# Kernel tuning notes

Measured on AMD Instinct MI355X. Metric: run time of the kernel, lower is better.

## Reference

```python
import jax, jax.numpy as jnp
import numpy as np
import math

D_MODEL = 512
D_FF = 4 * D_MODEL
N_EXPERTS = 8
VOCAB = 256
TOL = 0.15          # TeslaHarmonicGate tolerance
HARM = math.pi / 3.0  # harmonic spacing (Tesla 3-6-9 -> pi*k/3 harmonics over [-pi, pi])


def tesla_gate(angle):
    # Snap angle to the nearest harmonic (multiple of pi/3) when within tolerance.
    nearest = jnp.round(angle / HARM) * HARM
    return jnp.where(jnp.abs(angle - nearest) < TOL, nearest, angle)


def setup_inputs() -> dict:
    key = jax.random.key(0)
    ks = jax.random.split(key, 16)
    s = lambda d: 1.0 / np.sqrt(d)
    return {
        "byte_seq": jax.random.randint(ks[0], (4, 2048), 0, VOCAB, dtype=jnp.int32),
        "emb":    jax.random.normal(ks[1], (VOCAB, D_MODEL), jnp.float32) * 0.02,
        "phi_w":  jax.random.normal(ks[2], (D_MODEL, D_MODEL), jnp.float32) * s(D_MODEL),
        "phi_b":  jnp.zeros((D_MODEL,), jnp.float32),
        "amp_w":  jax.random.normal(ks[3], (D_MODEL, D_MODEL), jnp.float32) * s(D_MODEL),
        "amp_b":  jnp.zeros((D_MODEL,), jnp.float32),
        "gate_w": jax.random.normal(ks[4], (D_MODEL, N_EXPERTS), jnp.float32) * s(D_MODEL),
        "gate_b": jnp.zeros((N_EXPERTS,), jnp.float32),
        "w1":     jax.random.normal(ks[5], (N_EXPERTS, D_MODEL, D_FF), jnp.float32) * s(D_MODEL),
        "b1":     jnp.zeros((N_EXPERTS, D_FF), jnp.float32),
        "w2":     jax.random.normal(ks[6], (N_EXPERTS, D_FF, D_MODEL), jnp.float32) * s(D_FF),
        "b2":     jnp.zeros((N_EXPERTS, D_MODEL), jnp.float32),
        "head_w": jax.random.normal(ks[7], (D_MODEL, VOCAB), jnp.float32) * s(D_MODEL),
        "head_b": jnp.zeros((VOCAB,), jnp.float32),
    }


def _toroidal(x, phi_w, phi_b, amp_w, amp_b):
    # x: [B, T, C]; sequential toroidal recurrence over T via lax.scan.
    B, T, C = x.shape
    state0 = jnp.zeros((B, C), x.dtype)

    def step(state, xt):  # xt: [B, C]
        raw_angle = jnp.tanh(xt @ phi_w + phi_b) * jnp.pi
        angle = tesla_gate(raw_angle)
        new_state = jnp.cos(angle) * state - jnp.sin(angle) * (1.0 - state)
        new_state = jnp.clip(new_state, -1.0, 1.0)
        gated = jax.nn.sigmoid(xt @ amp_w + amp_b) * new_state
        return new_state, gated

    final_state, out = jax.lax.scan(step, state0, jnp.swapaxes(x, 0, 1))
    return jnp.swapaxes(out, 0, 1), final_state  # [B,T,C], [B,C]


def _moe(x, gate_w, gate_b, w1, b1, w2, b2):
    # Top-2 softmax routing with renormalized weights; per-expert FFN (GELU).
    B, T, C = x.shape
    xt = x.reshape(B * T, C)                        # [N, C]
    probs = jax.nn.softmax(xt @ gate_w + gate_b)    # [N, E]
    topw, topi = jax.lax.top_k(probs, 2)            # [N, 2]
    topw = topw / jnp.sum(topw, axis=-1, keepdims=True)
    out = jnp.zeros_like(xt)
    for e in range(N_EXPERTS):  # fixed small expert loop
        w_e = jnp.sum(jnp.where(topi == e, topw, 0.0), axis=-1)  # [N]
        h = jax.nn.gelu(xt @ w1[e] + b1[e])
        out = out + w_e[:, None] * (h @ w2[e] + b2[e])
    return out.reshape(B, T, C)


def reference(byte_seq, emb, phi_w, phi_b, amp_w, amp_b, gate_w, gate_b,
              w1, b1, w2, b2, head_w, head_b):
    x = emb[byte_seq]                                  # [B, T, C]
    x, next_state = _toroidal(x, phi_w, phi_b, amp_w, amp_b)
    moe_out = _moe(x, gate_w, gate_b, w1, b1, w2, b2)
    logits = moe_out @ head_w + head_b                 # [B, T, 256]
    return logits, next_state
```

## Files before the change

### kernel.cpp

```cpp
#include <hip/hip_runtime.h>
#include <hip/hip_fp16.h>
#include <math.h>


#define PI_F 3.14159265358979323846f
#define HARM_F 1.04719755119659774615f
#define INV_HARM_F 0.95492965855137201461f
#define TOL_F 0.15f

typedef float f32x16 __attribute__((ext_vector_type(16)));
typedef __bf16 bf16x8 __attribute__((ext_vector_type(8)));
typedef unsigned int u32x4 __attribute__((ext_vector_type(4)));
typedef unsigned int u32x2 __attribute__((ext_vector_type(2)));

__device__ __forceinline__ float bflo(unsigned u) { return __uint_as_float(u << 16); }
__device__ __forceinline__ float bfhi(unsigned u) { return __uint_as_float(u & 0xFFFF0000u); }
__device__ __forceinline__ unsigned short f2bf(float x) {
  unsigned u = __float_as_uint(x);
  unsigned r = (u + 0x7FFFu + ((u >> 16) & 1u)) >> 16;
  return (unsigned short)r;
}
__device__ __forceinline__ bf16x8 ld_frag(const void* p) {
  u32x4 v = *(const u32x4*)p;
  return __builtin_bit_cast(bf16x8, v);
}
__device__ __forceinline__ float tanh_fast(float z) {
  float zc = fminf(10.f, fmaxf(-10.f, z));
  float e2 = __expf(zc + zc);
  return (e2 - 1.f) / (e2 + 1.f);
}
__device__ __forceinline__ float sigmoid_fast(float z) {
  return 1.f / (1.f + __expf(-z));
}
__device__ __forceinline__ float gelu_tanh(float x) {
  float x3 = x * x * x;
  float t = 0.79788456080286535588f * (x + 0.044715f * x3);
  return 0.5f * x * (1.f + tanh_fast(t));
}
__device__ __forceinline__ void sincos_poly(float a, float* sn, float* cs) {
  float q = rintf(a * 0.63661977236758134f);
  int iq = (int)q;
  float t = fmaf(-q, 1.57079637050628662f, a);
  t = fmaf(q, 4.37113883e-8f, t);
  float t2 = t * t;
  float sp = t * fmaf(t2, fmaf(t2, fmaf(t2, -1.9515296e-4f, 8.3321609e-3f),
                               -1.6666654e-1f), 1.f);
  float cp = fmaf(t2 * t2,
                  fmaf(t2, fmaf(t2, 2.4433158e-5f, -1.3887316e-3f), 4.1666646e-2f),
                  fmaf(t2, -0.5f, 1.f));
  int m = iq & 3;
  bool swap = (m & 1) != 0;
  float ss = swap ? cp : sp;
  float cc = swap ? sp : cp;
  *sn = (m & 2) ? -ss : ss;
  *cs = ((m + 1) & 2) ? -cc : cc;
}

__global__ void k_embed2(const int* __restrict__ seq, const float* __restrict__ emb,
                         unsigned short* __restrict__ XhiP,
                         unsigned short* __restrict__ XloP) {
  int gid = blockIdx.x * 256 + threadIdx.x;
  int ent = gid >> 6, l = gid & 63;
  int tb = ent >> 5, ks = ent & 31;
  int tok = tb * 32 + (l & 31);
  int k0 = ks * 16 + (l >> 5) * 8;
  const float* src = emb + (size_t)seq[tok] * 512 + k0;
  float4 v0 = *(const float4*)src;
  float4 v1 = *(const float4*)(src + 4);
  float vv[8] = {v0.x, v0.y, v0.z, v0.w, v1.x, v1.y, v1.z, v1.w};
  unsigned h[8], lo[8];
#pragma unroll
  for (int j = 0; j < 8; ++j) {
    h[j] = f2bf(vv[j]);
    lo[j] = f2bf(vv[j] - bflo(h[j]));
  }
  u32x4 H, L;
  H.x = h[0] | (h[1] << 16);  H.y = h[2] | (h[3] << 16);
  H.z = h[4] | (h[5] << 16);  H.w = h[6] | (h[7] << 16);
  L.x = lo[0] | (lo[1] << 16); L.y = lo[2] | (lo[3] << 16);
  L.z = lo[4] | (lo[5] << 16); L.w = lo[6] | (lo[7] << 16);
  *(u32x4*)(XhiP + (size_t)ent * 512 + l * 8) = H;
  *(u32x4*)(XloP + (size_t)ent * 512 + l * 8) = L;
}

__global__ __launch_bounds__(256) void k_pack_b(const float* __restrict__ src, int ld,
                                                size_t srcE, unsigned short* __restrict__ dst,
                                                size_t dstE, int fragKtot) {
  __shared__ float Ls[512 * 33];
  int nb = blockIdx.x, kseg = blockIdx.y, e = blockIdx.z;
  const float* s = src + (size_t)e * srcE + (size_t)kseg * 512 * ld + nb * 32;
  unsigned short* d = dst + (size_t)e * dstE + ((size_t)(nb * fragKtot + kseg * 32)) * 512;
  int tid = threadIdx.x;
#pragma unroll
  for (int q = 0; q < 16; ++q) {
    int i = tid + q * 256;
    int row = i >> 3, c4 = i & 7;
    float4 v = *(const float4*)(s + (size_t)row * ld + c4 * 4);
    Ls[row * 33 + c4 * 4 + 0] = v.x;
    Ls[row * 33 + c4 * 4 + 1] = v.y;
    Ls[row * 33 + c4 * 4 + 2] = v.z;
    Ls[row * 33 + c4 * 4 + 3] = v.w;
  }
  __syncthreads();
#pragma unroll
  for (int q = 0; q < 8; ++q) {
    int i = tid + q * 256;
    int ks = i >> 6, l = i & 63;
    int col = l & 31, kb = (l >> 5) * 8 + ks * 16;
    u32x4 o;
    o.x = (unsigned)f2bf(Ls[(kb + 0) * 33 + col]) | ((unsigned)f2bf(Ls[(kb + 1) * 33 + col]) << 16);
    o.y = (unsigned)f2bf(Ls[(kb + 2) * 33 + col]) | ((unsigned)f2bf(Ls[(kb + 3) * 33 + col]) << 16);
    o.z = (unsigned)f2bf(Ls[(kb + 4) * 33 + col]) | ((unsigned)f2bf(Ls[(kb + 5) * 33 + col]) << 16);
    o.w = (unsigned)f2bf(Ls[(kb + 6) * 33 + col]) | ((unsigned)f2bf(Ls[(kb + 7) * 33 + col]) << 16);
    *(u32x4*)(d + (size_t)ks * 512 + l * 8) = o;
  }
}

__global__ __launch_bounds__(256, 3) void k_phi(
    const unsigned short* __restrict__ XhiP, const unsigned short* __restrict__ XloP,
    const float* __restrict__ phiW, const float* __restrict__ phiB,
    const float* __restrict__ ampW, const float* __restrict__ ampB,
    float* __restrict__ cosO, float* __restrict__ sinO, float* __restrict__ sigO) {
  __shared__ __align__(16) char wlds[2][8][1024];
  int tid = threadIdx.x;
  int w = tid >> 6, l = tid & 63;
  int l31 = l & 31, hi = l >> 5;
  int by = blockIdx.y;
  const float* Bsrc = (by < 4) ? phiW : ampW;
  const float* bias = (by < 4) ? phiB : ampB;
  int cb = (by & 3) * 128;

#define STAGE_W(KS, BUF)                                                        \
  {                                                                             \
    const float* wsrc = Bsrc + (size_t)((KS)*16 + hi * 8) * 512 + cb + w * 32 + l31; \
    float v0 = wsrc[0],    v1 = wsrc[512],  v2 = wsrc[1024], v3 = wsrc[1536];   \
    float v4 = wsrc[2048], v5 = wsrc[2560], v6 = wsrc[3072], v7 = wsrc[3584];   \
    unsigned h0 = f2bf(v0), h1 = f2bf(v1), h2 = f2bf(v2), h3 = f2bf(v3);        \
    unsigned h4 = f2bf(v4), h5 = f2bf(v5), h6 = f2bf(v6), h7 = f2bf(v7);        \
    u32x4 H, L;                                                                 \
    H.x = h0 | (h1 << 16); H.y = h2 | (h3 << 16);                               \
    H.z = h4 | (h5 << 16); H.w = h6 | (h7 << 16);                               \
    L.x = (unsigned)f2bf(v0 - bflo(h0)) | ((unsigned)f2bf(v1 - bflo(h1)) << 16); \
    L.y = (unsigned)f2bf(v2 - bflo(h2)) | ((unsigned)f2bf(v3 - bflo(h3)) << 16); \
    L.z = (unsigned)f2bf(v4 - bflo(h4)) | ((unsigned)f2bf(v5 - bflo(h5)) << 16); \
    L.w = (unsigned)f2bf(v6 - bflo(h6)) | ((unsigned)f2bf(v7 - bflo(h7)) << 16); \
    *(u32x4*)(&wlds[BUF][w * 2 + 0][l * 16]) = H;                               \
    *(u32x4*)(&wlds[BUF][w * 2 + 1][l * 16]) = L;                               \
  }

  int tb = blockIdx.x * 4 + w;
  const unsigned short* xh_base = XhiP + ((size_t)tb * 32) * 512 + l * 8;
  const unsigned short* xl_base = XloP + ((size_t)tb * 32) * 512 + l * 8;
  f32x16 a0, a1, a2, a3;
#pragma unroll
  for (int i = 0; i < 16; ++i) { a0[i] = 0.f; a1[i] = 0.f; a2[i] = 0.f; a3[i] = 0.f; }

  STAGE_W(0, 0);
  for (int ks = 0; ks < 32; ++ks) {
    __syncthreads();
    if (ks + 1 < 32) {
      if (((ks + 1) & 1) == 0) STAGE_W(ks + 1, 0) else STAGE_W(ks + 1, 1)
    }
    bf16x8 xh = *(const bf16x8*)(xh_base + (size_t)ks * 512);
    bf16x8 xl = *(const bf16x8*)(xl_base + (size_t)ks * 512);
    const char (*wb)[1024] = wlds[ks & 1];
    bf16x8 wh0 = ld_frag(&wb[0][l * 16]), wl0 = ld_frag(&wb[1][l * 16]);
    bf16x8 wh1 = ld_frag(&wb[2][l * 16]), wl1 = ld_frag(&wb[3][l * 16]);
    bf16x8 wh2 = ld_frag(&wb[4][l * 16]), wl2 = ld_frag(&wb[5][l * 16]);
    bf16x8 wh3 = ld_frag(&wb[6][l * 16]), wl3 = ld_frag(&wb[7][l * 16]);
    a0 = __builtin_amdgcn_mfma_f32_32x32x16_bf16(xh, wh0, a0, 0, 0, 0);
    a1 = __builtin_amdgcn_mfma_f32_32x32x16_bf16(xh, wh1, a1, 0, 0, 0);
    a2 = __builtin_amdgcn_mfma_f32_32x32x16_bf16(xh, wh2, a2, 0, 0, 0);
    a3 = __builtin_amdgcn_mfma_f32_32x32x16_bf16(xh, wh3, a3, 0, 0, 0);
    a0 = __builtin_amdgcn_mfma_f32_32x32x16_bf16(xl, wh0, a0, 0, 0, 0);
    a1 = __builtin_amdgcn_mfma_f32_32x32x16_bf16(xl, wh1, a1, 0, 0, 0);
    a2 = __builtin_amdgcn_mfma_f32_32x32x16_bf16(xl, wh2, a2, 0, 0, 0);
    a3 = __builtin_amdgcn_mfma_f32_32x32x16_bf16(xl, wh3, a3, 0, 0, 0);
    a0 = __builtin_amdgcn_mfma_f32_32x32x16_bf16(xh, wl0, a0, 0, 0, 0);
    a1 = __builtin_amdgcn_mfma_f32_32x32x16_bf16(xh, wl1, a1, 0, 0, 0);
    a2 = __builtin_amdgcn_mfma_f32_32x32x16_bf16(xh, wl2, a2, 0, 0, 0);
    a3 = __builtin_amdgcn_mfma_f32_32x32x16_bf16(xh, wl3, a3, 0, 0, 0);
  }

  int tokBase = blockIdx.x * 128 + w * 32;
#define PHI_EPI(ACC, NB)                                                        \
  {                                                                             \
    int c = cb + (NB)*32 + l31;                                                 \
    float bs = bias[c];                                                         \
    if (by < 4) {                                                               \
      _Pragma("unroll") for (int r = 0; r < 16; ++r) {                          \
        int tok = tokBase + (r & 3) + 8 * (r >> 2) + 4 * hi;                    \
        float z = ACC[r] + bs;                                                  \
        float a = tanh_fast(z) * PI_F;                                          \
        float nr = rintf(a * INV_HARM_F) * HARM_F;                              \
        if (fabsf(a - nr) < TOL_F) a = nr;                                      \
        float sn, cs;                                                           \
        sincos_poly(a, &sn, &cs);                                               \
        cosO[(size_t)tok * 512 + c] = cs;                                       \
        sinO[(size_t)tok * 512 + c] = sn;                                       \
      }                                                                         \
    } else {                                                                    \
      _Pragma("unroll") for (int r = 0; r < 16; ++r) {                          \
        int tok = tokBase + (r & 3) + 8 * (r >> 2) + 4 * hi;                    \
        sigO[(size_t)tok * 512 + c] = sigmoid_fast(ACC[r] + bs);                \
      }                                                                         \
    }                                                                           \
  }
  PHI_EPI(a0, 0)
  PHI_EPI(a1, 1)
  PHI_EPI(a2, 2)
  PHI_EPI(a3, 3)
}

__global__ __launch_bounds__(256, 1) void k_scan(const float* __restrict__ cosb,
                                                 const float* __restrict__ sinb,
                                                 const float* __restrict__ sigb,
                                                 float* __restrict__ xmoe,
                                                 float* __restrict__ nstate) {
  __shared__ float lds[2][3][64 * 64];
  int tid = threadIdx.x;
  int wv = tid >> 6, l = tid & 63;
  int b = blockIdx.x >> 3;
  int c0 = (blockIdx.x & 7) << 6;
  size_t base = ((size_t)b * 2048) * 512 + c0;

#define SCAN_STAGE(SRC, K, BUF)                                                \
  {                                                                            \
    float4 tmp[16];                                                            \
    size_t sb = base + ((size_t)(K) * 64 + tq) * 512 + cq * 4;                 \
    _Pragma("unroll") for (int t4 = 0; t4 < 16; ++t4)                          \
      tmp[t4] = *(const float4*)((SRC) + sb + (size_t)t4 * 4 * 512);           \
    _Pragma("unroll") for (int t4 = 0; t4 < 16; ++t4)                          \
      *(float4*)(&lds[BUF][wv - 1][(t4 * 4 + tq) * 64 + cq * 4]) = tmp[t4];    \
  }

  if (wv > 0) {
    const float* src = (wv == 1) ? cosb : (wv == 2) ? sinb : sigb;
    int tq = l >> 4, cq = l & 15;
    SCAN_STAGE(src, 0, 0);
    __syncthreads();
    for (int k = 0; k < 32; ++k) {
      if (k + 1 < 32) {
        if (((k + 1) & 1) == 0) SCAN_STAGE(src, k + 1, 0)
        else                    SCAN_STAGE(src, k + 1, 1)
      }
      __syncthreads();
    }
  } else {
    __syncthreads();
    float state = 0.f;
    for (int k = 0; k < 32; ++k) {
      const float* bufC = &lds[k & 1][0][0];
      const float* bufS = &lds[k & 1][1][0];
      const float* bufG = &lds[k & 1][2][0];
      size_t outb = base + (size_t)k * 64 * 512 + l;
#pragma unroll
      for (int tt = 0; tt < 64; ++tt) {
        float pc = bufC[tt * 64 + l];
        float ps = bufS[tt * 64 + l];
        float pg = bufG[tt * 64 + l];
        float st = fmaf(pc + ps, state, -ps);
        st = fminf(1.f, fmaxf(-1.f, st));
        state = st;
        xmoe[outb + (size_t)tt * 512] = pg * st;
      }
      __syncthreads();
    }
    nstate[(size_t)b * 512 + c0 + l] = state;
  }
}

__global__ __launch_bounds__(256) void k_gate(const float* __restrict__ xmoe,
                                              const float* __restrict__ gw_g,
                                              const float* __restrict__ gb,
                                              int* __restrict__ e01p,
                                              unsigned* __restrict__ w01p) {
  __shared__ float gw[4096];
  int tid = threadIdx.x;
  for (int i = tid; i < 4096; i += 256) gw[i] = gw_g[i];
  __syncthreads();
  int tok = blockIdx.x * 32 + (tid >> 3);
  int e = tid & 7;
  float acc = gb[e];
  const float4* xr = (const float4*)(xmoe + (size_t)tok * 512);
  for (int k4 = 0; k4 < 128; ++k4) {
    float4 x = xr[k4];
    acc += x.x * gw[(k4 * 4 + 0) * 8 + e];
    acc += x.y * gw[(k4 * 4 + 1) * 8 + e];
    acc += x.z * gw[(k4 * 4 + 2) * 8 + e];
    acc += x.w * gw[(k4 * 4 + 3) * 8 + e];
  }
  float m = acc;
  m = fmaxf(m, __shfl_xor(m, 1));
  m = fmaxf(m, __shfl_xor(m, 2));
  m = fmaxf(m, __shfl_xor(m, 4));
  float p = expf(acc - m);
  float ss = p;
  ss += __shfl_xor(ss, 1); ss += __shfl_xor(ss, 2); ss += __shfl_xor(ss, 4);
  p /= ss;
  float v1 = p; int i1 = e;
  {
    float ov; int oi;
    ov = __shfl_xor(v1, 1); oi = __shfl_xor(i1, 1);
    if (ov > v1 || (ov == v1 && oi < i1)) { v1 = ov; i1 = oi; }
    ov = __shfl_xor(v1, 2); oi = __shfl_xor(i1, 2);
    if (ov > v1 || (ov == v1 && oi < i1)) { v1 = ov; i1 = oi; }
    ov = __shfl_xor(v1, 4); oi = __shfl_xor(i1, 4);
    if (ov > v1 || (ov == v1 && oi < i1)) { v1 = ov; i1 = oi; }
  }
  float v2 = (e == i1) ? -1.f : p; int i2 = e;
  {
    float ov; int oi;
    ov = __shfl_xor(v2, 1); oi = __shfl_xor(i2, 1);
    if (ov > v2 || (ov == v2 && oi < i2)) { v2 = ov; i2 = oi; }
    ov = __shfl_xor(v2, 2); oi = __shfl_xor(i2, 2);
    if (ov > v2 || (ov == v2 && oi < i2)) { v2 = ov; i2 = oi; }
    ov = __shfl_xor(v2, 4); oi = __shfl_xor(i2, 4);
    if (ov > v2 || (ov == v2 && oi < i2)) { v2 = ov; i2 = oi; }
  }
  if (e == 0) {
    float s2 = v1 + v2;
    __half h1 = __float2half(v1 / s2), h2 = __float2half(v2 / s2);
    e01p[tok] = i1 | (i2 << 8);
    w01p[tok] = (unsigned)__half_as_ushort(h1) | ((unsigned)__half_as_ushort(h2) << 16);
  }
}

__global__ void k_build(const int* __restrict__ e01p, const unsigned* __restrict__ w01p,
                        int* __restrict__ list, float* __restrict__ wlist,
                        int* __restrict__ counts, int* __restrict__ eoff,
                        int* __restrict__ tokpos, int* __restrict__ tmap) {
  __shared__ int cnt[8], cur[8];
  int tid = threadIdx.x, lane = tid & 63;
  if (tid < 8) cnt[tid] = 0;
  __syncthreads();
  for (int i = tid; i < 16384; i += 256) {
    int tok = i >> 1, j = i & 1;
    int ee = (e01p[tok] >> (8 * j)) & 255;
#pragma unroll
    for (int x = 0; x < 8; ++x) {
      unsigned long long m = __ballot(ee == x);
      if (m != 0ull && lane == (__ffsll((long long)m) - 1)) atomicAdd(&cnt[x], __popcll(m));
    }
  }
  __syncthreads();
  if (tid == 0) {
    int s = 0;
#pragma unroll
    for (int x = 0; x < 8; ++x) {
      cur[x] = s; eoff[x] = s; counts[x] = cnt[x]; s += cnt[x];
    }
  }
  __syncthreads();
  for (int i = tid; i < 272; i += 256) tmap[i] = -1;
  __syncthreads();
  if (tid == 0) {
    int ntiles = 0, tstart[8];
#pragma unroll
    for (int e = 0; e < 8; ++e) { tstart[e] = ntiles; ntiles += (cnt[e] + 95) / 96; }
    int q = ntiles >> 3, r = ntiles & 7;
    for (int e = 0; e < 8; ++e) {
      int nt = (cnt[e] + 95) / 96;
      for (int t = 0; t < nt; ++t) {
        int k = tstart[e] + t;
        int c, o;
        if (k < r * (q + 1)) { c = k / (q + 1); o = k - c * (q + 1); }
        else { int k2 = k - r * (q + 1); c = r + k2 / q; o = k2 - (k2 / q) * q; }
        tmap[8 * o + c] = (e << 16) | t;
      }
    }
  }
  __syncthreads();
  for (int i = tid; i < 16384; i += 256) {
    int tok = i >> 1, j = i & 1;
    int ee = (e01p[tok] >> (8 * j)) & 255;
    unsigned wp = w01p[tok];
    unsigned short us = (unsigned short)(j ? (wp >> 16) : (wp & 0xFFFFu));
    float w = __half2float(__ushort_as_half(us));
    int pos = 0;
#pragma unroll
    for (int x = 0; x < 8; ++x) {
      unsigned long long m = __ballot(ee == x);
      if (m == 0ull) continue;
      int leader = __ffsll((long long)m) - 1;
      int bb = 0;
      if (lane == leader) bb = atomicAdd(&cur[x], __popcll(m));
      bb = __shfl(bb, leader);
      if (ee == x) pos = bb + __popcll(m & ((1ull << lane) - 1ull));
    }
    list[pos] = tok;
    wlist[pos] = w;
    tokpos[i] = pos;
  }
}

#define HS_OFF 98304

__global__ __launch_bounds__(512, 2) void k_ffn(
    const float* __restrict__ xmoe, const int* __restrict__ list,
    const float* __restrict__ wlist, const int* __restrict__ counts,
    const int* __restrict__ eoff, const int* __restrict__ tmap,
    const unsigned short* __restrict__ W1Pk, const float* __restrict__ b1g,
    const unsigned short* __restrict__ W2Pk, const float* __restrict__ b2g,
    unsigned short* __restrict__ Yb) {
  int mp = tmap[blockIdx.x];
  if (mp < 0) return;
  int e = mp >> 16, tile = mp & 0xFFFF;
  int cnt = counts[e];
  int base = eoff[e] + tile * 96;
  int valid = cnt - tile * 96;
  if (valid > 96) valid = 96;
  __shared__ __align__(16) char smem[147456];
  __shared__ int toks[96];
  __shared__ float wts[96];
  int tid = threadIdx.x;
  int w = tid >> 6, l = tid & 63;
  int l31 = l & 31, hi = l >> 5;
  if (tid < 96) {
    int idx = tile * 96 + tid;
    bool v = idx < cnt;
    toks[tid] = list[eoff[e] + (v ? idx : 0)];
    wts[tid] = v ? wlist[eoff[e] + idx] : 0.f;
  }
  __syncthreads();
#pragma unroll
  for (int s = 0; s < 12; ++s) {
    int sl = s * 512 + tid;
    int ent = sl >> 6, ll = sl & 63;
    int ks = ent / 3, t3 = ent - ks * 3;
    int tok = toks[t3 * 32 + (ll & 31)];
    const float* src = xmoe + (size_t)tok * 512 + ks * 16 + (ll >> 5) * 8;
    float4 v0 = *(const float4*)src;
    float4 v1 = *(const float4*)(src + 4);
    u32x4 u;
    u.x = (unsigned)f2bf(v0.x) | ((unsigned)f2bf(v0.y) << 16);
    u.y = (unsigned)f2bf(v0.z) | ((unsigned)f2bf(v0.w) << 16);
    u.z = (unsigned)f2bf(v1.x) | ((unsigned)f2bf(v1.y) << 16);
    u.w = (unsigned)f2bf(v1.z) | ((unsigned)f2bf(v1.w) << 16);
    *(u32x4*)(smem + ent * 1024 + ll * 16) = u;
  }
  f32x16 acc00, acc01, acc02, acc10, acc11, acc12;
#pragma unroll
  for (int i = 0; i < 16; ++i) {
    acc00[i] = 0.f; acc01[i] = 0.f; acc02[i] = 0.f;
    acc10[i] = 0.f; acc11[i] = 0.f; acc12[i] = 0.f;
  }
  __syncthreads();

  const size_t dstE1 = (size_t)64 * 32 * 512;
  const size_t dstE2 = (size_t)16 * 128 * 512;
  for (int it = 0; it < 8; ++it) {
    f32x16 z0, z1, z2;
#pragma unroll
    for (int i = 0; i < 16; ++i) { z0[i] = 0.f; z1[i] = 0.f; z2[i] = 0.f; }
    const unsigned short* w1p =
        W1Pk + (size_t)e * dstE1 + ((size_t)(it * 8 + w) * 32) * 512 + l * 8;
#pragma unroll 8
    for (int ks = 0; ks < 32; ++ks) {
      bf16x8 a = *(const bf16x8*)(w1p + (size_t)ks * 512);
      bf16x8 b0 = ld_frag(smem + (ks * 3 + 0) * 1024 + l * 16);
      bf16x8 b1 = ld_frag(smem + (ks * 3 + 1) * 1024 + l * 16);
      bf16x8 b2 = ld_frag(smem + (ks * 3 + 2) * 1024 + l * 16);
      z0 = __builtin_amdgcn_mfma_f32_32x32x16_bf16(a, b0, z0, 0, 0, 0);
      z1 = __builtin_amdgcn_mfma_f32_32x32x16_bf16(a, b1, z1, 0, 0, 0);
      z2 = __builtin_amdgcn_mfma_f32_32x32x16_bf16(a, b2, z2, 0, 0, 0);
    }
#define GELU_STORE(Z, T3)                                                       \
  {                                                                             \
    _Pragma("unroll") for (int rq = 0; rq < 4; ++rq) {                          \
      int fb = w * 32 + 8 * rq + 4 * hi;                                        \
      float4 bv = *(const float4*)(b1g + e * 2048 + it * 256 + fb);             \
      float g0 = gelu_tanh(Z[4 * rq + 0] + bv.x);                               \
      float g1 = gelu_tanh(Z[4 * rq + 1] + bv.y);                               \
      float g2 = gelu_tanh(Z[4 * rq + 2] + bv.z);                               \
      float g3 = gelu_tanh(Z[4 * rq + 3] + bv.w);                               \
      u32x2 p;                                                                  \
      p.x = (unsigned)f2bf(g0) | ((unsigned)f2bf(g1) << 16);                    \
      p.y = (unsigned)f2bf(g2) | ((unsigned)f2bf(g3) << 16);                    \
      int ent = (w * 2 + (rq >> 1)) * 3 + (T3);                                 \
      int lanep = l31 + 32 * (rq & 1);                                          \
      *(u32x2*)(smem + HS_OFF + ent * 1024 + lanep * 16 + hi * 8) = p;          \
    }                                                                           \
  }
    GELU_STORE(z0, 0)
    GELU_STORE(z1, 1)
    GELU_STORE(z2, 2)
    __syncthreads();
    const unsigned short* w2a =
        W2Pk + (size_t)e * dstE2 + ((size_t)(w * 2) * 128 + it * 16) * 512 + l * 8;
    const unsigned short* w2b = w2a + (size_t)128 * 512;
#pragma unroll 8
    for (int fs = 0; fs < 16; ++fs) {
      bf16x8 a0 = *(const bf16x8*)(w2a + (size_t)fs * 512);
      bf16x8 a1 = *(const bf16x8*)(w2b + (size_t)fs * 512);
      bf16x8 h0 = ld_frag(smem + HS_OFF + (fs * 3 + 0) * 1024 + l * 16);
      bf16x8 h1 = ld_frag(smem + HS_OFF + (fs * 3 + 1) * 1024 + l * 16);
      bf16x8 h2 = ld_frag(smem + HS_OFF + (fs * 3 + 2) * 1024 + l * 16);
      acc00 = __builtin_amdgcn_mfma_f32_32x32x16_bf16(a0, h0, acc00, 0, 0, 0);
      acc01 = __builtin_amdgcn_mfma_f32_32x32x16_bf16(a0, h1, acc01, 0, 0, 0);
      acc02 = __builtin_amdgcn_mfma_f32_32x32x16_bf16(a0, h2, acc02, 0, 0, 0);
      acc10 = __builtin_amdgcn_mfma_f32_32x32x16_bf16(a1, h0, acc10, 0, 0, 0);
      acc11 = __builtin_amdgcn_mfma_f32_32x32x16_bf16(a1, h1, acc11, 0, 0, 0);
      acc12 = __builtin_amdgcn_mfma_f32_32x32x16_bf16(a1, h2, acc12, 0, 0, 0);
    }
    __syncthreads();
  }
#define EPI_STORE(ACC, JC, T3)                                                  \
  {                                                                             \
    _Pragma("unroll") for (int rq = 0; rq < 4; ++rq) {                          \
      int c0 = (w * 2 + (JC)) * 32 + 8 * rq + 4 * hi;                           \
      float4 b2v = *(const float4*)(b2g + e * 512 + c0);                        \
      int tok = (T3)*32 + l31;                                                  \
      float wt = wts[tok];                                                      \
      u32x2 p;                                                                  \
      p.x = (unsigned)f2bf((ACC[4 * rq + 0] + b2v.x) * wt) |                    \
            ((unsigned)f2bf((ACC[4 * rq + 1] + b2v.y) * wt) << 16);             \
      p.y = (unsigned)f2bf((ACC[4 * rq + 2] + b2v.z) * wt) |                    \
            ((unsigned)f2bf((ACC[4 * rq + 3] + b2v.w) * wt) << 16);             \
      *(u32x2*)(smem + tok * 1024 + ((c0 * 2) ^ ((tok & 7) << 4))) = p;         \
    }                                                                           \
  }
  EPI_STORE(acc00, 0, 0)
  EPI_STORE(acc01, 0, 1)
  EPI_STORE(acc02, 0, 2)
  EPI_STORE(acc10, 1, 0)
  EPI_STORE(acc11, 1, 1)
  EPI_STORE(acc12, 1, 2)
  __syncthreads();
#pragma unroll
  for (int s = 0; s < 12; ++s) {
    int i = tid + s * 512;
    int row = i >> 6, g = i & 63;
    if (row < valid) {
      u32x4 v = *(u32x4*)(smem + row * 1024 + ((g * 16) ^ ((row & 7) << 4)));
      *(u32x4*)(Yb + (size_t)(base + row) * 512 + g * 8) = v;
    }
  }
}

__global__ __launch_bounds__(256) void k_head(const unsigned short* __restrict__ Yb,
                                              const int* __restrict__ tokpos,
                                              const unsigned short* __restrict__ headPk,
                                              const float* __restrict__ headB,
                                              float* __restrict__ out) {
  __shared__ __align__(16) char As[16384];
  __shared__ int tp[256];
  int tid = threadIdx.x;
  int w = tid >> 6, l = tid & 63;
  int l31 = l & 31, hi = l >> 5;
  int mg = w & 1, ng = w >> 1;
  int bm = blockIdx.x * 128, by = blockIdx.y;
  tp[tid] = tokpos[bm * 2 + tid];
  f32x16 acc00, acc01, acc10, acc11;
#pragma unroll
  for (int i = 0; i < 16; ++i) { acc00[i] = 0.f; acc01[i] = 0.f; acc10[i] = 0.f; acc11[i] = 0.f; }
  int nblk0 = by * 4 + ng * 2;
  __syncthreads();
  for (int kb = 0; kb < 8; ++kb) {
#pragma unroll
    for (int s = 0; s < 4; ++s) {
      int i = tid + s * 256;
      int row = i >> 3, g = i & 7;
      int p1 = tp[row * 2], p2 = tp[row * 2 + 1];
      u32x4 va = *(const u32x4*)(Yb + (size_t)p1 * 512 + kb * 64 + g * 8);
      u32x4 vb = *(const u32x4*)(Yb + (size_t)p2 * 512 + kb * 64 + g * 8);
      u32x4 o;
      o.x = (unsigned)f2bf(bflo(va.x) + bflo(vb.x)) | ((unsigned)f2bf(bfhi(va.x) + bfhi(vb.x)) << 16);
      o.y = (unsigned)f2bf(bflo(va.y) + bflo(vb.y)) | ((unsigned)f2bf(bfhi(va.y) + bfhi(vb.y)) << 16);
      o.z = (unsigned)f2bf(bflo(va.z) + bflo(vb.z)) | ((unsigned)f2bf(bfhi(va.z) + bfhi(vb.z)) << 16);
      o.w = (unsigned)f2bf(bflo(va.w) + bflo(vb.w)) | ((unsigned)f2bf(bfhi(va.w) + bfhi(vb.w)) << 16);
      *(u32x4*)(As + row * 128 + ((g * 16) ^ ((row & 7) << 4))) = o;
    }
    __syncthreads();
#pragma unroll
    for (int ks = 0; ks < 4; ++ks) {
      int r0 = mg * 64 + l31, r1 = r0 + 32;
      int kbyte = ks * 32 + hi * 16;
      bf16x8 a0 = ld_frag(As + r0 * 128 + (kbyte ^ ((r0 & 7) << 4)));
      bf16x8 a1 = ld_frag(As + r1 * 128 + (kbyte ^ ((r1 & 7) << 4)));
      const unsigned short* hp = headPk + ((size_t)nblk0 * 32 + kb * 4 + ks) * 512 + l * 8;
      bf16x8 b0 = *(const bf16x8*)hp;
      bf16x8 b1 = *(const bf16x8*)(hp + 32 * 512);
      acc00 = __builtin_amdgcn_mfma_f32_32x32x16_bf16(a0, b0, acc00, 0, 0, 0);
      acc01 = __builtin_amdgcn_mfma_f32_32x32x16_bf16(a0, b1, acc01, 0, 0, 0);
      acc10 = __builtin_amdgcn_mfma_f32_32x32x16_bf16(a1, b0, acc10, 0, 0, 0);
      acc11 = __builtin_amdgcn_mfma_f32_32x32x16_bf16(a1, b1, acc11, 0, 0, 0);
    }
    __syncthreads();
  }
#pragma unroll
  for (int mf = 0; mf < 2; ++mf) {
#pragma unroll
    for (int nf = 0; nf < 2; ++nf) {
      int nc = by * 128 + ng * 64 + nf * 32 + l31;
      float hb = headB[nc];
#pragma unroll
      for (int r = 0; r < 16; ++r) {
        int m = bm + mg * 64 + mf * 32 + (r & 3) + 8 * (r >> 2) + 4 * hi;
        float v;
        if (mf == 0) v = (nf == 0) ? acc00[r] : acc01[r];
        else         v = (nf == 0) ? acc10[r] : acc11[r];
        out[(size_t)m * 256 + nc] = v + hb;
      }
    }
  }
}

extern "C" void kernel_launch(void* const* d_in, const int* in_sizes, int n_in,
                              void* d_out, int out_size, void* d_ws, size_t ws_size,
                              hipStream_t stream) {
  (void)in_sizes; (void)n_in; (void)out_size; (void)ws_size;
  const int* seq     = (const int*)d_in[0];
  const float* emb   = (const float*)d_in[1];
  const float* phi_w = (const float*)d_in[2];
  const float* phi_b = (const float*)d_in[3];
  const float* amp_w = (const float*)d_in[4];
  const float* amp_b = (const float*)d_in[5];
  const float* gate_w = (const float*)d_in[6];
  const float* gate_b = (const float*)d_in[7];
  const float* w1 = (const float*)d_in[8];
  const float* b1 = (const float*)d_in[9];
  const float* w2 = (const float*)d_in[10];
  const float* b2 = (const float*)d_in[11];
  const float* head_w = (const float*)d_in[12];
  const float* head_b = (const float*)d_in[13];
  float* out = (float*)d_out;

  char* ws = (char*)d_ws;
  const size_t BUF = 16777216;
  float* X    = (float*)(ws);
  float* COSb = (float*)(ws + BUF);
  float* SINb = (float*)(ws + 2 * BUF);
  float* SIGb = (float*)(ws + 3 * BUF);
  unsigned short* XhiP = (unsigned short*)X;
  unsigned short* XloP = XhiP + (size_t)8192 * 512;
  unsigned short* Yb   = (unsigned short*)COSb;
  unsigned short* W1Pk = (unsigned short*)SINb;
  unsigned short* W2Pk = (unsigned short*)SIGb;
  char* sm = ws + 4 * BUF;
  int*      e01p   = (int*)(sm);
  unsigned* w01p   = (unsigned*)(sm + 32768);
  int*      list   = (int*)(sm + 65536);
  float*    wlist  = (float*)(sm + 131072);
  int*      tokpos = (int*)(sm + 196608);
  int*      counts = (int*)(sm + 262144);
  int*      eoff   = (int*)(sm + 262144 + 64);
  unsigned short* headPk = (unsigned short*)(sm + 266240);
  int*      tmap   = (int*)(sm + 266240 + 262144);

  k_embed2<<<2048, 256, 0, stream>>>(seq, emb, XhiP, XloP);
  k_pack_b<<<dim3(8, 1, 1), 256, 0, stream>>>(head_w, 256, 0, headPk, 0, 32);
  k_phi<<<dim3(64, 8), 256, 0, stream>>>(XhiP, XloP, phi_w, phi_b, amp_w, amp_b,
                                         COSb, SINb, SIGb);
  k_scan<<<32, 256, 0, stream>>>(COSb, SINb, SIGb, X, out + 2097152);
  k_pack_b<<<dim3(64, 1, 8), 256, 0, stream>>>(w1, 2048, (size_t)512 * 2048, W1Pk,
                                               (size_t)64 * 32 * 512, 32);
  k_pack_b<<<dim3(16, 4, 8), 256, 0, stream>>>(w2, 512, (size_t)2048 * 512, W2Pk,
                                               (size_t)16 * 128 * 512, 128);
  k_gate<<<256, 256, 0, stream>>>(X, gate_w, gate_b, e01p, w01p);
  k_build<<<1, 256, 0, stream>>>(e01p, w01p, list, wlist, counts, eoff, tokpos, tmap);
  k_ffn<<<192, 512, 0, stream>>>(X, list, wlist, counts, eoff, tmap,
                                 W1Pk, b1, W2Pk, b2, Yb);
  k_head<<<dim3(64, 2), 256, 0, stream>>>(Yb, tokpos, headPk, head_b, out);
}
```

Before: 393.5 us.

## Split MoE FFN token groups across wave pairs with 1024-thread blocks

The expert FFN kernel now launches 1024 threads per block instead of 512, pairing waves so each pair splits the three 32-token groups. One wave handles two groups in the first GEMM and one in the second, and the other wave takes the opposite split, which balances MFMA work. The aim is to double resident waves per CU and cut per-wave accumulator registers, improving latency hiding on a grid of only 192 blocks. In exchange, each weight fragment is now loaded from global memory by both waves of a pair, and barriers now synchronize twice as many waves.

```diff
diff --git a/kernel.cpp b/kernel.cpp
--- a/kernel.cpp
+++ b/kernel.cpp
@@ -396,7 +396,7 @@
 
 #define HS_OFF 98304
 
-__global__ __launch_bounds__(512, 2) void k_ffn(
+__global__ __launch_bounds__(1024, 4) void k_ffn(
     const float* __restrict__ xmoe, const int* __restrict__ list,
     const float* __restrict__ wlist, const int* __restrict__ counts,
     const int* __restrict__ eoff, const int* __restrict__ tmap,
@@ -416,6 +416,7 @@
   int tid = threadIdx.x;
   int w = tid >> 6, l = tid & 63;
   int l31 = l & 31, hi = l >> 5;
+  int grp = w >> 1, fg = w & 1;
   if (tid < 96) {
     int idx = tile * 96 + tid;
     bool v = idx < cnt;
@@ -424,8 +425,8 @@
   }
   __syncthreads();
 #pragma unroll
-  for (int s = 0; s < 12; ++s) {
-    int sl = s * 512 + tid;
+  for (int s = 0; s < 6; ++s) {
+    int sl = s * 1024 + tid;
     int ent = sl >> 6, ll = sl & 63;
     int ks = ent / 3, t3 = ent - ks * 3;
     int tok = toks[t3 * 32 + (ll & 31)];
@@ -439,36 +440,15 @@
     u.w = (unsigned)f2bf(v1.z) | ((unsigned)f2bf(v1.w) << 16);
     *(u32x4*)(smem + ent * 1024 + ll * 16) = u;
   }
-  f32x16 acc00, acc01, acc02, acc10, acc11, acc12;
-#pragma unroll
-  for (int i = 0; i < 16; ++i) {
-    acc00[i] = 0.f; acc01[i] = 0.f; acc02[i] = 0.f;
-    acc10[i] = 0.f; acc11[i] = 0.f; acc12[i] = 0.f;
-  }
   __syncthreads();
 
   const size_t dstE1 = (size_t)64 * 32 * 512;
   const size_t dstE2 = (size_t)16 * 128 * 512;
-  for (int it = 0; it < 8; ++it) {
-    f32x16 z0, z1, z2;
-#pragma unroll
-    for (int i = 0; i < 16; ++i) { z0[i] = 0.f; z1[i] = 0.f; z2[i] = 0.f; }
-    const unsigned short* w1p =
-        W1Pk + (size_t)e * dstE1 + ((size_t)(it * 8 + w) * 32) * 512 + l * 8;
-#pragma unroll 8
-    for (int ks = 0; ks < 32; ++ks) {
-      bf16x8 a = *(const bf16x8*)(w1p + (size_t)ks * 512);
-      bf16x8 b0 = ld_frag(smem + (ks * 3 + 0) * 1024 + l * 16);
-      bf16x8 b1 = ld_frag(smem + (ks * 3 + 1) * 1024 + l * 16);
-      bf16x8 b2 = ld_frag(smem + (ks * 3 + 2) * 1024 + l * 16);
-      z0 = __builtin_amdgcn_mfma_f32_32x32x16_bf16(a, b0, z0, 0, 0, 0);
-      z1 = __builtin_amdgcn_mfma_f32_32x32x16_bf16(a, b1, z1, 0, 0, 0);
-      z2 = __builtin_amdgcn_mfma_f32_32x32x16_bf16(a, b2, z2, 0, 0, 0);
-    }
+
 #define GELU_STORE(Z, T3)                                                       \
   {                                                                             \
     _Pragma("unroll") for (int rq = 0; rq < 4; ++rq) {                          \
-      int fb = w * 32 + 8 * rq + 4 * hi;                                        \
+      int fb = grp * 32 + 8 * rq + 4 * hi;                                      \
       float4 bv = *(const float4*)(b1g + e * 2048 + it * 256 + fb);             \
       float g0 = gelu_tanh(Z[4 * rq + 0] + bv.x);                               \
       float g1 = gelu_tanh(Z[4 * rq + 1] + bv.y);                               \
@@ -477,38 +457,15 @@
       u32x2 p;                                                                  \
       p.x = (unsigned)f2bf(g0) | ((unsigned)f2bf(g1) << 16);                    \
       p.y = (unsigned)f2bf(g2) | ((unsigned)f2bf(g3) << 16);                    \
-      int ent = (w * 2 + (rq >> 1)) * 3 + (T3);                                 \
+      int ent = (grp * 2 + (rq >> 1)) * 3 + (T3);                               \
       int lanep = l31 + 32 * (rq & 1);                                          \
       *(u32x2*)(smem + HS_OFF + ent * 1024 + lanep * 16 + hi * 8) = p;          \
     }                                                                           \
   }
-    GELU_STORE(z0, 0)
-    GELU_STORE(z1, 1)
-    GELU_STORE(z2, 2)
-    __syncthreads();
-    const unsigned short* w2a =
-        W2Pk + (size_t)e * dstE2 + ((size_t)(w * 2) * 128 + it * 16) * 512 + l * 8;
-    const unsigned short* w2b = w2a + (size_t)128 * 512;
-#pragma unroll 8
-    for (int fs = 0; fs < 16; ++fs) {
-      bf16x8 a0 = *(const bf16x8*)(w2a + (size_t)fs * 512);
-      bf16x8 a1 = *(const bf16x8*)(w2b + (size_t)fs * 512);
-      bf16x8 h0 = ld_frag(smem + HS_OFF + (fs * 3 + 0) * 1024 + l * 16);
-      bf16x8 h1 = ld_frag(smem + HS_OFF + (fs * 3 + 1) * 1024 + l * 16);
-      bf16x8 h2 = ld_frag(smem + HS_OFF + (fs * 3 + 2) * 1024 + l * 16);
-      acc00 = __builtin_amdgcn_mfma_f32_32x32x16_bf16(a0, h0, acc00, 0, 0, 0);
-      acc01 = __builtin_amdgcn_mfma_f32_32x32x16_bf16(a0, h1, acc01, 0, 0, 0);
-      acc02 = __builtin_amdgcn_mfma_f32_32x32x16_bf16(a0, h2, acc02, 0, 0, 0);
-      acc10 = __builtin_amdgcn_mfma_f32_32x32x16_bf16(a1, h0, acc10, 0, 0, 0);
-      acc11 = __builtin_amdgcn_mfma_f32_32x32x16_bf16(a1, h1, acc11, 0, 0, 0);
-      acc12 = __builtin_amdgcn_mfma_f32_32x32x16_bf16(a1, h2, acc12, 0, 0, 0);
-    }
-    __syncthreads();
-  }
 #define EPI_STORE(ACC, JC, T3)                                                  \
   {                                                                             \
     _Pragma("unroll") for (int rq = 0; rq < 4; ++rq) {                          \
-      int c0 = (w * 2 + (JC)) * 32 + 8 * rq + 4 * hi;                           \
+      int c0 = (grp * 2 + (JC)) * 32 + 8 * rq + 4 * hi;                         \
       float4 b2v = *(const float4*)(b2g + e * 512 + c0);                        \
       int tok = (T3)*32 + l31;                                                  \
       float wt = wts[tok];                                                      \
@@ -520,16 +477,86 @@
       *(u32x2*)(smem + tok * 1024 + ((c0 * 2) ^ ((tok & 7) << 4))) = p;         \
     }                                                                           \
   }
-  EPI_STORE(acc00, 0, 0)
-  EPI_STORE(acc01, 0, 1)
-  EPI_STORE(acc02, 0, 2)
-  EPI_STORE(acc10, 1, 0)
-  EPI_STORE(acc11, 1, 1)
-  EPI_STORE(acc12, 1, 2)
-  __syncthreads();
-#pragma unroll
-  for (int s = 0; s < 12; ++s) {
-    int i = tid + s * 512;
+
+  if (fg == 0) {
+    f32x16 acc02, acc12;
+#pragma unroll
+    for (int i = 0; i < 16; ++i) { acc02[i] = 0.f; acc12[i] = 0.f; }
+    for (int it = 0; it < 8; ++it) {
+      f32x16 z0, z1;
+#pragma unroll
+      for (int i = 0; i < 16; ++i) { z0[i] = 0.f; z1[i] = 0.f; }
+      const unsigned short* w1p =
+          W1Pk + (size_t)e * dstE1 + ((size_t)(it * 8 + grp) * 32) * 512 + l * 8;
+#pragma unroll 8
+      for (int ks = 0; ks < 32; ++ks) {
+        bf16x8 a = *(const bf16x8*)(w1p + (size_t)ks * 512);
+        bf16x8 b0 = ld_frag(smem + (ks * 3 + 0) * 1024 + l * 16);
+        bf16x8 b1 = ld_frag(smem + (ks * 3 + 1) * 1024 + l * 16);
+        z0 = __builtin_amdgcn_mfma_f32_32x32x16_bf16(a, b0, z0, 0, 0, 0);
+        z1 = __builtin_amdgcn_mfma_f32_32x32x16_bf16(a, b1, z1, 0, 0, 0);
+      }
+      GELU_STORE(z0, 0)
+      GELU_STORE(z1, 1)
+      __syncthreads();
+      const unsigned short* w2a =
+          W2Pk + (size_t)e * dstE2 + ((size_t)(grp * 2) * 128 + it * 16) * 512 + l * 8;
+      const unsigned short* w2b = w2a + (size_t)128 * 512;
+#pragma unroll 8
+      for (int fs = 0; fs < 16; ++fs) {
+        bf16x8 a0 = *(const bf16x8*)(w2a + (size_t)fs * 512);
+        bf16x8 a1 = *(const bf16x8*)(w2b + (size_t)fs * 512);
+        bf16x8 h2 = ld_frag(smem + HS_OFF + (fs * 3 + 2) * 1024 + l * 16);
+        acc02 = __builtin_amdgcn_mfma_f32_32x32x16_bf16(a0, h2, acc02, 0, 0, 0);
+        acc12 = __builtin_amdgcn_mfma_f32_32x32x16_bf16(a1, h2, acc12, 0, 0, 0);
+      }
+      __syncthreads();
+    }
+    EPI_STORE(acc02, 0, 2)
+    EPI_STORE(acc12, 1, 2)
+  } else {
+    f32x16 acc00, acc01, acc10, acc11;
+#pragma unroll
+    for (int i = 0; i < 16; ++i) { acc00[i] = 0.f; acc01[i] = 0.f; acc10[i] = 0.f; acc11[i] = 0.f; }
+    for (int it = 0; it < 8; ++it) {
+      f32x16 z2;
+#pragma unroll
+      for (int i = 0; i < 16; ++i) z2[i] = 0.f;
+      const unsigned short* w1p =
+          W1Pk + (size_t)e * dstE1 + ((size_t)(it * 8 + grp) * 32) * 512 + l * 8;
+#pragma unroll 8
+      for (int ks = 0; ks < 32; ++ks) {
+        bf16x8 a = *(const bf16x8*)(w1p + (size_t)ks * 512);
+        bf16x8 b2 = ld_frag(smem + (ks * 3 + 2) * 1024 + l * 16);
+        z2 = __builtin_amdgcn_mfma_f32_32x32x16_bf16(a, b2, z2, 0, 0, 0);
+      }
+      GELU_STORE(z2, 2)
+      __syncthreads();
+      const unsigned short* w2a =
+          W2Pk + (size_t)e * dstE2 + ((size_t)(grp * 2) * 128 + it * 16) * 512 + l * 8;
+      const unsigned short* w2b = w2a + (size_t)128 * 512;
+#pragma unroll 8
+      for (int fs = 0; fs < 16; ++fs) {
+        bf16x8 a0 = *(const bf16x8*)(w2a + (size_t)fs * 512);
+        bf16x8 a1 = *(const bf16x8*)(w2b + (size_t)fs * 512);
+        bf16x8 h0 = ld_frag(smem + HS_OFF + (fs * 3 + 0) * 1024 + l * 16);
+        bf16x8 h1 = ld_frag(smem + HS_OFF + (fs * 3 + 1) * 1024 + l * 16);
+        acc00 = __builtin_amdgcn_mfma_f32_32x32x16_bf16(a0, h0, acc00, 0, 0, 0);
+        acc01 = __builtin_amdgcn_mfma_f32_32x32x16_bf16(a0, h1, acc01, 0, 0, 0);
+        acc10 = __builtin_amdgcn_mfma_f32_32x32x16_bf16(a1, h0, acc10, 0, 0, 0);
+        acc11 = __builtin_amdgcn_mfma_f32_32x32x16_bf16(a1, h1, acc11, 0, 0, 0);
+      }
+      __syncthreads();
+    }
+    EPI_STORE(acc00, 0, 0)
+    EPI_STORE(acc01, 0, 1)
+    EPI_STORE(acc10, 1, 0)
+    EPI_STORE(acc11, 1, 1)
+  }
+  __syncthreads();
+#pragma unroll
+  for (int s = 0; s < 6; ++s) {
+    int i = tid + s * 1024;
     int row = i >> 6, g = i & 63;
     if (row < valid) {
       u32x4 v = *(u32x4*)(smem + row * 1024 + ((g * 16) ^ ((row & 7) << 4)));
@@ -659,7 +686,7 @@
                                                (size_t)16 * 128 * 512, 128);
   k_gate<<<256, 256, 0, stream>>>(X, gate_w, gate_b, e01p, w01p);
   k_build<<<1, 256, 0, stream>>>(e01p, w01p, list, wlist, counts, eoff, tokpos, tmap);
-  k_ffn<<<192, 512, 0, stream>>>(X, list, wlist, counts, eoff, tmap,
-                                 W1Pk, b1, W2Pk, b2, Yb);
+  k_ffn<<<192, 1024, 0, stream>>>(X, list, wlist, counts, eoff, tmap,
+                                  W1Pk, b1, W2Pk, b2, Yb);
   k_head<<<dim3(64, 2), 256, 0, stream>>>(Yb, tokpos, headPk, head_b, out);
 }
```

New measurement: 409.6 us. 1.04x slower.
